# Kernel optimization log

Hardware: AMD Instinct MI355X
Metric: run time of the kernel (lower is better)

Reference implementation:

```python
import jax, jax.numpy as jnp
import numpy as np

D_IN = 128
D_K = 100
SCALE = float(np.sqrt(100.0))


def setup_inputs() -> dict:
    key = jax.random.key(0)
    ks = jax.random.split(key, 8)
    S = 8192
    x1 = jax.random.uniform(ks[0], (S, D_IN), dtype=jnp.float32)
    x2 = jax.random.uniform(ks[1], (S, D_IN), dtype=jnp.float32)
    # Linear params (PyTorch Linear: y = x @ W.T + b); stored here pre-transposed as [in, out]
    lim = 1.0 / np.sqrt(D_IN)
    Wq = jax.random.uniform(ks[2], (D_IN, D_K), jnp.float32, -lim, lim)
    bq = jax.random.uniform(ks[3], (D_K,), jnp.float32, -lim, lim)
    Wk = jax.random.uniform(ks[4], (D_IN, D_K), jnp.float32, -lim, lim)
    bk = jax.random.uniform(ks[5], (D_K,), jnp.float32, -lim, lim)
    Wv = jax.random.uniform(ks[6], (D_IN, D_K), jnp.float32, -lim, lim)
    bv = jax.random.uniform(ks[7], (D_K,), jnp.float32, -lim, lim)
    return {"x1": x1, "x2": x2, "Wq": Wq, "bq": bq, "Wk": Wk, "bk": bk, "Wv": Wv, "bv": bv}


def reference(x1, x2, Wq, bq, Wk, bk, Wv, bv):
    # Q/K/V projections
    q = x1 @ Wq + bq          # [S, D_K]
    k = x2 @ Wk + bk          # [S, D_K]
    v = x2 @ Wv + bv          # [S, D_K]
    # scaled dot-product attention (single head); dropout is identity (eval mode)
    scores = jnp.einsum('qd,kd->qk', q, k) / SCALE   # [S, S]
    attn = jax.nn.softmax(scores, axis=-1)
    return attn @ v            # [S, D_K]
```

## Files before the change

kernel.cpp:

```cpp
#include <hip/hip_runtime.h>
#include <hip/hip_bf16.h>


typedef __bf16 bf16x8 __attribute__((ext_vector_type(8)));
typedef float  f32x4  __attribute__((ext_vector_type(4)));
typedef short  short8_t __attribute__((ext_vector_type(8)));

#define SM_C 0.14426950408889634f

#if __has_builtin(__builtin_amdgcn_global_load_lds)
#define HAVE_GLL 1
#endif

__device__ __forceinline__ void gload16(const short* g, short* l){
#ifdef HAVE_GLL
  __builtin_amdgcn_global_load_lds(
      (__attribute__((address_space(1))) void*)g,
      (__attribute__((address_space(3))) void*)l,
      16, 0, 0);
#else
  *(short8_t*)(l + (threadIdx.x & 63)*8) = *(const short8_t*)(g);
#endif
}

__device__ __forceinline__ short bf(float f){ return __builtin_bit_cast(short, (__bf16)f); }
__device__ __forceinline__ float bf2f(unsigned short v){
  unsigned u = ((unsigned)v) << 16;
  return __builtin_bit_cast(float, u);
}

#define VMW(n) asm volatile("s_waitcnt vmcnt(" #n ")" ::: "memory")
#define BARC do{ __builtin_amdgcn_s_barrier(); asm volatile("" ::: "memory"); }while(0)

__global__ __launch_bounds__(256) void proj_qkv(
    const float* __restrict__ x1, const float* __restrict__ x2,
    const float* __restrict__ Wq, const float* __restrict__ bq,
    const float* __restrict__ Wk, const float* __restrict__ bk,
    const float* __restrict__ Wv, const float* __restrict__ bv,
    short* __restrict__ qg, short* __restrict__ kg, short* __restrict__ vT2)
{
  __shared__ float xs[16][128];
  __shared__ float vs[16][104];
  const int z = blockIdx.y;
  const float* x = (z == 0) ? x1 : x2;
  const float* W = (z == 0) ? Wq : (z == 1) ? Wk : Wv;
  const float* b = (z == 0) ? bq : (z == 1) ? bk : bv;
  const int rb = blockIdx.x << 4;
  const int t  = threadIdx.x;
  for (int i = t; i < 2048; i += 256) xs[i >> 7][i & 127] = x[(rb << 7) + i];
  __syncthreads();
  const int rw = t >> 5, cs = t & 31;
  float4 a0 = make_float4(0.f,0.f,0.f,0.f), a1 = a0;
  if (cs < 25){
    a0 = *(const float4*)(b + (cs << 2)); a1 = a0;
#pragma unroll 8
    for (int i = 0; i < 128; ++i){
      const float4 wv = *(const float4*)(W + i*100 + (cs << 2));
      const float xv0 = xs[rw][i], xv1 = xs[rw+8][i];
      a0.x = fmaf(xv0, wv.x, a0.x); a0.y = fmaf(xv0, wv.y, a0.y);
      a0.z = fmaf(xv0, wv.z, a0.z); a0.w = fmaf(xv0, wv.w, a0.w);
      a1.x = fmaf(xv1, wv.x, a1.x); a1.y = fmaf(xv1, wv.y, a1.y);
      a1.z = fmaf(xv1, wv.z, a1.z); a1.w = fmaf(xv1, wv.w, a1.w);
    }
  }
  if (z < 2){
    if (z == 0){
      a0.x*=SM_C; a0.y*=SM_C; a0.z*=SM_C; a0.w*=SM_C;
      a1.x*=SM_C; a1.y*=SM_C; a1.z*=SM_C; a1.w*=SM_C;
    }
    short* o = (z == 0) ? qg : kg;
    if (cs < 25){
      short4 h0, h1;
      h0.x=bf(a0.x); h0.y=bf(a0.y); h0.z=bf(a0.z); h0.w=bf(a0.w);
      h1.x=bf(a1.x); h1.y=bf(a1.y); h1.z=bf(a1.z); h1.w=bf(a1.w);
      *(short4*)(o + ((rb + rw)     << 7) + (cs << 2)) = h0;
      *(short4*)(o + ((rb + rw + 8) << 7) + (cs << 2)) = h1;
    } else {
      short4 hz; hz.x=0; hz.y=0; hz.z=0; hz.w=0;
      *(short4*)(o + ((rb + rw)     << 7) + 100 + ((cs - 25) << 2)) = hz;
      *(short4*)(o + ((rb + rw + 8) << 7) + 100 + ((cs - 25) << 2)) = hz;
    }
  } else {
    if (cs < 25){
      vs[rw  ][(cs<<2)+0]=a0.x; vs[rw  ][(cs<<2)+1]=a0.y; vs[rw  ][(cs<<2)+2]=a0.z; vs[rw  ][(cs<<2)+3]=a0.w;
      vs[rw+8][(cs<<2)+0]=a1.x; vs[rw+8][(cs<<2)+1]=a1.y; vs[rw+8][(cs<<2)+2]=a1.z; vs[rw+8][(cs<<2)+3]=a1.w;
    }
    __syncthreads();
    if (t < 128){
      const int d = t;
#pragma unroll
      for (int h = 0; h < 4; ++h){
        const int kv0 = rb + h*4;
        const int o32 = kv0 & 31;
        const int idx = (o32 < 16) ? ((o32 >> 2) << 3) : ((((o32 - 16) >> 2) << 3) + 4);
        const int r0 = kv0 - rb;
        short4 hv;
        hv.x = (d<100)? bf(vs[r0+0][d]) : (d==100 ? (short)0x3F80 : (short)0);
        hv.y = (d<100)? bf(vs[r0+1][d]) : (d==100 ? (short)0x3F80 : (short)0);
        hv.z = (d<100)? bf(vs[r0+2][d]) : (d==100 ? (short)0x3F80 : (short)0);
        hv.w = (d<100)? bf(vs[r0+3][d]) : (d==100 ? (short)0x3F80 : (short)0);
        *(short4*)(vT2 + (d << 13) + (kv0 & ~31) + idx) = hv;
      }
    }
  }
}

__global__ __launch_bounds__(256, 2) void attn_fwd(
    const short* __restrict__ qg, const short* __restrict__ kg,
    const short* __restrict__ vT2, short* __restrict__ pacc,
    float* __restrict__ lsumg)
{
  __shared__ alignas(1024) short sK[2][4096];
  __shared__ alignas(1024) short sVT[2][4096];
  const int tid  = threadIdx.x;
  const int w    = tid >> 6;
  const int lane = tid & 63;
  const int g    = lane >> 4;
  const int ln   = lane & 15;
  const int orig = blockIdx.x;
  const int part = ((orig & 7) << 1) | ((orig >> 3) & 1);
  const int qt   = orig >> 4;
  const int qb   = qt*256 + w*64;
  const int kvbase = part << 9;

  bf16x8 qf[4][4];
#pragma unroll
  for (int sub = 0; sub < 4; ++sub)
#pragma unroll
    for (int ks = 0; ks < 4; ++ks)
      qf[sub][ks] = *(const bf16x8*)(qg + (qb + sub*16 + ln)*128 + ks*32 + g*8);

  f32x4 acc[4][7];
#pragma unroll
  for (int sub = 0; sub < 4; ++sub)
#pragma unroll
    for (int db = 0; db < 7; ++db) acc[sub][db] = f32x4{0.f,0.f,0.f,0.f};

  const short *kA0, *kA1, *vA0, *vA1;
  {
    const int r0 = (w << 2)       + (lane >> 4);
    const int r1 = ((w + 4) << 2) + (lane >> 4);
    kA0 = kg + (kvbase + r0)*128 + (((lane & 15) ^ (r0 & 15)) << 3);
    kA1 = kg + (kvbase + r1)*128 + (((lane & 15) ^ (r1 & 15)) << 3);
    const int a0 = (w << 10) + (lane << 4);
    const int a1 = ((w + 4) << 10) + (lane << 4);
    const int dd0 = a0 >> 7, d0 = (dd0 << 1) + ((a0 >> 6) & 1), gs0 = ((a0 >> 4) & 3) ^ (dd0 & 3);
    const int dd1 = a1 >> 7, d1 = (dd1 << 1) + ((a1 >> 6) & 1), gs1 = ((a1 >> 4) & 3) ^ (dd1 & 3);
    vA0 = vT2 + d0*8192 + kvbase + (gs0 << 3);
    vA1 = vT2 + d1*8192 + kvbase + (gs1 << 3);
  }

  auto stageK = [&](int tt){
    short* dst = sK[tt & 1];
    const int off = tt << 12;
    gload16(kA0 + off, dst + (w << 9));
    gload16(kA1 + off, dst + ((w + 4) << 9));
  };
  auto stageV = [&](int tt){
    short* dst = sVT[tt & 1];
    const int off = tt << 5;
    gload16(vA0 + off, dst + (w << 9));
    gload16(vA1 + off, dst + ((w + 4) << 9));
  };

  bf16x8 pb[4];

  auto phaseA = [&](int buf, int sv){
    if (sv >= 0) stageV(sv);
    const short* sKc = sK[buf];
    f32x4 st[4][2];
#pragma unroll
    for (int sub = 0; sub < 4; ++sub){
      st[sub][0] = f32x4{0.f,0.f,0.f,0.f};
      st[sub][1] = f32x4{0.f,0.f,0.f,0.f};
    }
    __builtin_amdgcn_s_setprio(1);
#pragma unroll
    for (int s = 0; s < 2; ++s){
      const int rbase = (s*16 + ln) << 7;
#pragma unroll
      for (int ks = 0; ks < 4; ++ks){
        bf16x8 kf = *(const bf16x8*)(sKc + rbase + ((((ks << 2) + g) ^ ln) << 3));
        st[0][s] = __builtin_amdgcn_mfma_f32_16x16x32_bf16(kf, qf[0][ks], st[0][s], 0, 0, 0);
        st[1][s] = __builtin_amdgcn_mfma_f32_16x16x32_bf16(kf, qf[1][ks], st[1][s], 0, 0, 0);
        st[2][s] = __builtin_amdgcn_mfma_f32_16x16x32_bf16(kf, qf[2][ks], st[2][s], 0, 0, 0);
        st[3][s] = __builtin_amdgcn_mfma_f32_16x16x32_bf16(kf, qf[3][ks], st[3][s], 0, 0, 0);
      }
    }
    __builtin_amdgcn_s_setprio(0);
#pragma unroll
    for (int sub = 0; sub < 4; ++sub){
      bf16x8 pv;
#pragma unroll
      for (int r = 0; r < 4; ++r){
        pv[r]     = (__bf16)exp2f(st[sub][0][r]);
        pv[4 + r] = (__bf16)exp2f(st[sub][1][r]);
      }
      pb[sub] = pv;
    }
  };

  auto phaseB = [&](int buf, int sk){
    if (sk >= 0) stageK(sk);
    const short* sVc = sVT[buf];
    __builtin_amdgcn_s_setprio(1);
#pragma unroll
    for (int db = 0; db < 7; ++db){
      const int row = db*16 + ln;
      const int dd  = row >> 1;
      bf16x8 vf = *(const bf16x8*)(sVc + (dd << 6) + ((row & 1) << 5) + ((g ^ (dd & 3)) << 3));
      acc[0][db] = __builtin_amdgcn_mfma_f32_16x16x32_bf16(vf, pb[0], acc[0][db], 0, 0, 0);
      acc[1][db] = __builtin_amdgcn_mfma_f32_16x16x32_bf16(vf, pb[1], acc[1][db], 0, 0, 0);
      acc[2][db] = __builtin_amdgcn_mfma_f32_16x16x32_bf16(vf, pb[2], acc[2][db], 0, 0, 0);
      acc[3][db] = __builtin_amdgcn_mfma_f32_16x16x32_bf16(vf, pb[3], acc[3][db], 0, 0, 0);
    }
    __builtin_amdgcn_s_setprio(0);
  };

  stageK(0); stageV(0); stageK(1);
  for (int t = 0; t < 14; ++t){
    VMW(4); BARC; phaseA(t & 1, t + 1);
    VMW(4); BARC; phaseB(t & 1, t + 2);
  }
  VMW(4); BARC; phaseA(0, 15);
  VMW(4); BARC; phaseB(0, -1);
  VMW(2); BARC; phaseA(1, -1);
  VMW(0); BARC; phaseB(1, -1);

#pragma unroll
  for (int sub = 0; sub < 4; ++sub){
#pragma unroll
    for (int db = 0; db < 7; ++db)
#pragma unroll
      for (int r = 0; r < 4; ++r){
        const int d = db*16 + g*4 + r;
        if (d < 100)
          pacc[((part*100 + d) << 13) + qb + sub*16 + ln] = bf(acc[sub][db][r]);
      }
    if (g == 1)
      lsumg[(part << 13) + qb + sub*16 + ln] = acc[sub][6][0];
  }
}

__global__ __launch_bounds__(256) void merge_parts(
    const short* __restrict__ pacc, const float* __restrict__ lsumg,
    float* __restrict__ out)
{
  __shared__ float ol[64][26];
  const int t   = threadIdx.x;
  const int qo8 = (t & 7) << 3;
  const int dt  = t >> 3;
  const int qb  = blockIdx.x << 6;
  const int db  = blockIdx.y * 25;
  const int q0  = qb + qo8;

  float L8[8];
#pragma unroll
  for (int j = 0; j < 8; ++j) L8[j] = 0.f;
#pragma unroll
  for (int p = 0; p < 16; ++p){
    const float4 a = *(const float4*)(lsumg + (p << 13) + q0);
    const float4 c = *(const float4*)(lsumg + (p << 13) + q0 + 4);
    L8[0]+=a.x; L8[1]+=a.y; L8[2]+=a.z; L8[3]+=a.w;
    L8[4]+=c.x; L8[5]+=c.y; L8[6]+=c.z; L8[7]+=c.w;
  }

  if (dt < 25){
    const int d = db + dt;
    float s8[8];
#pragma unroll
    for (int j = 0; j < 8; ++j) s8[j] = 0.f;
#pragma unroll
    for (int p = 0; p < 16; ++p){
      short8_t v = *(const short8_t*)(pacc + ((p*100 + d) << 13) + q0);
#pragma unroll
      for (int j = 0; j < 8; ++j) s8[j] += bf2f((unsigned short)v[j]);
    }
#pragma unroll
    for (int j = 0; j < 8; ++j) ol[qo8 + j][dt] = s8[j] / L8[j];
  }
  __syncthreads();
  for (int idx = t; idx < 1600; idx += 256){
    const int q2 = idx / 25, d2 = idx - q2*25;
    out[(qb + q2)*100 + db + d2] = ol[q2][d2];
  }
}

extern "C" void kernel_launch(void* const* d_in, const int* in_sizes, int n_in,
                              void* d_out, int out_size, void* d_ws, size_t ws_size,
                              hipStream_t stream)
{
  const float* x1 = (const float*)d_in[0];
  const float* x2 = (const float*)d_in[1];
  const float* Wq = (const float*)d_in[2];
  const float* bq = (const float*)d_in[3];
  const float* Wk = (const float*)d_in[4];
  const float* bk = (const float*)d_in[5];
  const float* Wv = (const float*)d_in[6];
  const float* bv = (const float*)d_in[7];
  char* ws = (char*)d_ws;
  short* qg    = (short*)ws;
  short* kg    = (short*)(ws + (1u << 21));
  short* vT2   = (short*)(ws + (2u << 21));
  short* pacc  = (short*)(ws + (3u << 21));
  float* lsumg = (float*)(ws + (3u << 21) + 26214400u);
  float* out   = (float*)d_out;

  proj_qkv<<<dim3(512, 3), 256, 0, stream>>>(x1, x2, Wq, bq, Wk, bk, Wv, bv, qg, kg, vT2);
  attn_fwd<<<512, 256, 0, stream>>>(qg, kg, vT2, pacc, lsumg);
  merge_parts<<<dim3(128, 4), 256, 0, stream>>>(pacc, lsumg, out);
}
```

Baseline: 77.86 us.

## Double-pair K/V staging with one barrier per two KV tiles

Result: no change. 78.65 us (+1.0%).

```diff
diff --git a/kernel.cpp b/kernel.cpp
--- a/kernel.cpp
+++ b/kernel.cpp
@@ -110,8 +110,8 @@
     const short* __restrict__ vT2, short* __restrict__ pacc,
     float* __restrict__ lsumg)
 {
-  __shared__ alignas(1024) short sK[2][4096];
-  __shared__ alignas(1024) short sVT[2][4096];
+  __shared__ alignas(1024) short sK[4][4096];
+  __shared__ alignas(1024) short sVT[4][4096];
   const int tid  = threadIdx.x;
   const int w    = tid >> 6;
   const int lane = tid & 63;
@@ -150,23 +150,21 @@
     vA1 = vT2 + d1*8192 + kvbase + (gs1 << 3);
   }
 
-  auto stageK = [&](int tt){
-    short* dst = sK[tt & 1];
-    const int off = tt << 12;
-    gload16(kA0 + off, dst + (w << 9));
-    gload16(kA1 + off, dst + ((w + 4) << 9));
+  auto stagePair = [&](int tt){
+#pragma unroll
+    for (int u = 0; u < 2; ++u){
+      const int tu = tt + u;
+      short* dk = sK[tu & 3];
+      gload16(kA0 + (tu << 12), dk + (w << 9));
+      gload16(kA1 + (tu << 12), dk + ((w + 4) << 9));
+      short* dv = sVT[tu & 3];
+      gload16(vA0 + (tu << 5), dv + (w << 9));
+      gload16(vA1 + (tu << 5), dv + ((w + 4) << 9));
+    }
   };
-  auto stageV = [&](int tt){
-    short* dst = sVT[tt & 1];
-    const int off = tt << 5;
-    gload16(vA0 + off, dst + (w << 9));
-    gload16(vA1 + off, dst + ((w + 4) << 9));
-  };
-
-  bf16x8 pb[4];
-
-  auto phaseA = [&](int buf, int sv){
-    if (sv >= 0) stageV(sv);
+
+  auto computeTile = [&](int tt){
+    const int buf = tt & 3;
     const short* sKc = sK[buf];
     f32x4 st[4][2];
 #pragma unroll
@@ -188,6 +186,7 @@
       }
     }
     __builtin_amdgcn_s_setprio(0);
+    bf16x8 pb[4];
 #pragma unroll
     for (int sub = 0; sub < 4; ++sub){
       bf16x8 pv;
@@ -198,10 +197,6 @@
       }
       pb[sub] = pv;
     }
-  };
-
-  auto phaseB = [&](int buf, int sk){
-    if (sk >= 0) stageK(sk);
     const short* sVc = sVT[buf];
     __builtin_amdgcn_s_setprio(1);
 #pragma unroll
@@ -217,15 +212,15 @@
     __builtin_amdgcn_s_setprio(0);
   };
 
-  stageK(0); stageV(0); stageK(1);
-  for (int t = 0; t < 14; ++t){
-    VMW(4); BARC; phaseA(t & 1, t + 1);
-    VMW(4); BARC; phaseB(t & 1, t + 2);
-  }
-  VMW(4); BARC; phaseA(0, 15);
-  VMW(4); BARC; phaseB(0, -1);
-  VMW(2); BARC; phaseA(1, -1);
-  VMW(0); BARC; phaseB(1, -1);
+  stagePair(0);
+#pragma unroll 1
+  for (int wd = 0; wd < 8; ++wd){
+    VMW(0);
+    BARC;
+    if (wd < 7) stagePair(2*wd + 2);
+    computeTile(2*wd);
+    computeTile(2*wd + 1);
+  }
 
 #pragma unroll
   for (int sub = 0; sub < 4; ++sub){
```

## Fuse split-KV merge into attention kernel via grid-wide atomic barrier

Applied to the files above, without the earlier changes.

After: 233.3 us. +199.6%, slower.

```diff
diff --git a/kernel.cpp b/kernel.cpp
--- a/kernel.cpp
+++ b/kernel.cpp
@@ -108,7 +108,8 @@
 __global__ __launch_bounds__(256, 2) void attn_fwd(
     const short* __restrict__ qg, const short* __restrict__ kg,
     const short* __restrict__ vT2, short* __restrict__ pacc,
-    float* __restrict__ lsumg)
+    float* __restrict__ lsumg, unsigned* __restrict__ ctr,
+    float* __restrict__ out)
 {
   __shared__ alignas(1024) short sK[2][4096];
   __shared__ alignas(1024) short sVT[2][4096];
@@ -240,49 +241,46 @@
     if (g == 1)
       lsumg[(part << 13) + qb + sub*16 + ln] = acc[sub][6][0];
   }
-}
-
-__global__ __launch_bounds__(256) void merge_parts(
-    const short* __restrict__ pacc, const float* __restrict__ lsumg,
-    float* __restrict__ out)
-{
-  __shared__ float ol[64][26];
-  const int t   = threadIdx.x;
-  const int qo8 = (t & 7) << 3;
-  const int dt  = t >> 3;
-  const int qb  = blockIdx.x << 6;
-  const int db  = blockIdx.y * 25;
-  const int q0  = qb + qo8;
-
-  float L8[8];
-#pragma unroll
-  for (int j = 0; j < 8; ++j) L8[j] = 0.f;
-#pragma unroll
-  for (int p = 0; p < 16; ++p){
-    const float4 a = *(const float4*)(lsumg + (p << 13) + q0);
-    const float4 c = *(const float4*)(lsumg + (p << 13) + q0 + 4);
-    L8[0]+=a.x; L8[1]+=a.y; L8[2]+=a.z; L8[3]+=a.w;
-    L8[4]+=c.x; L8[5]+=c.y; L8[6]+=c.z; L8[7]+=c.w;
-  }
-
-  if (dt < 25){
-    const int d = db + dt;
-    float s8[8];
-#pragma unroll
-    for (int j = 0; j < 8; ++j) s8[j] = 0.f;
-#pragma unroll
-    for (int p = 0; p < 16; ++p){
-      short8_t v = *(const short8_t*)(pacc + ((p*100 + d) << 13) + q0);
-#pragma unroll
-      for (int j = 0; j < 8; ++j) s8[j] += bf2f((unsigned short)v[j]);
-    }
-#pragma unroll
-    for (int j = 0; j < 8; ++j) ol[qo8 + j][dt] = s8[j] / L8[j];
-  }
+
+  __threadfence();
   __syncthreads();
-  for (int idx = t; idx < 1600; idx += 256){
-    const int q2 = idx / 25, d2 = idx - q2*25;
-    out[(qb + q2)*100 + db + d2] = ol[q2][d2];
+  if (tid == 0){
+    __hip_atomic_fetch_add(ctr, 1u, __ATOMIC_RELEASE, __HIP_MEMORY_SCOPE_AGENT);
+    unsigned v = 0; long it = 0;
+    do {
+      v = __hip_atomic_load(ctr, __ATOMIC_ACQUIRE, __HIP_MEMORY_SCOPE_AGENT);
+    } while (v < 512u && ++it < (1L << 26));
+  }
+  __syncthreads();
+  __threadfence();
+
+  {
+    float* linv = (float*)&sK[0][0];
+    const int q0 = orig << 4;
+    if (tid < 16){
+      float L = 0.f;
+#pragma unroll
+      for (int p = 0; p < 16; ++p) L += lsumg[(p << 13) + q0 + tid];
+      linv[tid] = 1.0f / L;
+    }
+    __syncthreads();
+    if (tid < 200){
+      const int d    = tid >> 1;
+      const int half = tid & 1;
+      const int q8   = q0 + (half << 3);
+      float s8[8];
+#pragma unroll
+      for (int j = 0; j < 8; ++j) s8[j] = 0.f;
+#pragma unroll
+      for (int p = 0; p < 16; ++p){
+        short8_t v = *(const short8_t*)(pacc + ((p*100 + d) << 13) + q8);
+#pragma unroll
+        for (int j = 0; j < 8; ++j) s8[j] += bf2f((unsigned short)v[j]);
+      }
+#pragma unroll
+      for (int j = 0; j < 8; ++j)
+        out[(q8 + j)*100 + d] = s8[j] * linv[(half << 3) + j];
+    }
   }
 }
 
@@ -299,14 +297,15 @@
   const float* Wv = (const float*)d_in[6];
   const float* bv = (const float*)d_in[7];
   char* ws = (char*)d_ws;
-  short* qg    = (short*)ws;
-  short* kg    = (short*)(ws + (1u << 21));
-  short* vT2   = (short*)(ws + (2u << 21));
-  short* pacc  = (short*)(ws + (3u << 21));
-  float* lsumg = (float*)(ws + (3u << 21) + 26214400u);
-  float* out   = (float*)d_out;
-
+  short*    qg    = (short*)ws;
+  short*    kg    = (short*)(ws + (1u << 21));
+  short*    vT2   = (short*)(ws + (2u << 21));
+  short*    pacc  = (short*)(ws + (3u << 21));
+  float*    lsumg = (float*)(ws + (3u << 21) + 26214400u);
+  unsigned* ctr   = (unsigned*)(ws + (3u << 21) + 26214400u + 524288u);
+  float*    out   = (float*)d_out;
+
+  hipMemsetAsync(ctr, 0, 4, stream);
   proj_qkv<<<dim3(512, 3), 256, 0, stream>>>(x1, x2, Wq, bq, Wk, bk, Wv, bv, qg, kg, vT2);
-  attn_fwd<<<512, 256, 0, stream>>>(qg, kg, vT2, pacc, lsumg);
-  merge_parts<<<dim3(128, 4), 256, 0, stream>>>(pacc, lsumg, out);
-}
+  attn_fwd<<<512, 256, 0, stream>>>(qg, kg, vT2, pacc, lsumg, ctr, out);
+}
```
